# Optimization experiments

Measured on AMD Instinct MI355X. Metric: run time of the kernel, lower is better.

Reference implementation:

```python
import jax, jax.numpy as jnp
import numpy as np

T, H, I, E, TOP_K = 4096, 2048, 1024, 16, 2
I_SHARED = 1024  # moe_intermediate_size * n_shared_experts


def _silu_and_mul(gu):
    g, u = jnp.split(gu, 2, axis=-1)
    return jax.nn.silu(g) * u


def setup_inputs() -> dict:
    key = jax.random.key(0)
    ks = jax.random.split(key, 8)
    s = 0.02
    return {
        "hidden_states": jax.random.normal(ks[0], (T, H), jnp.float32),
        "gate_w": jax.random.normal(ks[1], (E, H), jnp.float32) * s,          # router
        "w1": jax.random.normal(ks[2], (E, 2 * I, H), jnp.float32) * s,       # expert gate_up
        "b1": jax.random.normal(ks[3], (E, 2 * I), jnp.float32) * s,
        "w2": jax.random.normal(ks[4], (E, H, I), jnp.float32) * s,           # expert down
        "sg_w": jax.random.normal(ks[5], (2 * I_SHARED, H), jnp.float32) * s, # shared gate_up
        "sg_b": jax.random.normal(ks[6], (2 * I_SHARED,), jnp.float32) * s,
        "sd_w": jax.random.normal(ks[7], (H, I_SHARED), jnp.float32) * s,     # shared down
    }


def reference(hidden_states, gate_w, w1, b1, w2, sg_w, sg_b, sd_w):
    x = hidden_states  # [T, H]

    # shared expert MLP (gate_up has bias, down does not)
    shared = _silu_and_mul(x @ sg_w.T + sg_b) @ sd_w.T  # [T, H]

    # router: softmax -> top-k -> renormalize (norm_topk_prob=True)
    probs = jax.nn.softmax(x @ gate_w.T, axis=-1)       # [T, E]
    wts, idx = jax.lax.top_k(probs, TOP_K)              # [T, k]
    wts = wts / jnp.sum(wts, axis=-1, keepdims=True)

    # per-expert combine coefficient: coef[e, t] = sum_k wts[t,k] * (idx[t,k]==e)
    coef = jnp.sum(jax.nn.one_hot(idx, E, dtype=x.dtype) * wts[..., None], axis=1).T  # [E, T]

    def body(acc, params):
        w1e, b1e, w2e, ce = params
        a = _silu_and_mul(x @ w1e.T + b1e)   # [T, I]
        return acc + ce[:, None] * (a @ w2e.T), None

    out, _ = jax.lax.scan(body, jnp.zeros_like(x), (w1, b1, w2, coef))
    return out + shared
```

## Files before the change

### kernel.cpp

```cpp
#include <hip/hip_runtime.h>
#include <hip/hip_bf16.h>
#include <stdint.h>

#define T_TOK 4096
#define H_DIM 2048
#define I_DIM 1024
#define NEXP  16
#define NROWS 16384

typedef short bf16x8 __attribute__((ext_vector_type(8)));
typedef float f32x4  __attribute__((ext_vector_type(4)));
typedef unsigned short u16;

__device__ __forceinline__ u16 f2b(float f) {
  union { __hip_bfloat16 h; u16 u; } cv;
  cv.h = __float2bfloat16(f);
  return cv.u;
}

__device__ __forceinline__ void gload16(const void* g, void* l) {
  __builtin_amdgcn_global_load_lds((const __attribute__((address_space(1))) void*)g,
                                   (__attribute__((address_space(3))) void*)l, 16, 0, 0);
}

__device__ __forceinline__ bf16x8 cvt_frag2(const float* pLo, const float* pHi) {
  f32x4 v0 = *(const f32x4*)pLo;
  f32x4 v1 = *(const f32x4*)pHi;
  bf16x8 o;
  o[0] = (short)f2b(v0[0]); o[1] = (short)f2b(v0[1]);
  o[2] = (short)f2b(v0[2]); o[3] = (short)f2b(v0[3]);
  o[4] = (short)f2b(v1[0]); o[5] = (short)f2b(v1[1]);
  o[6] = (short)f2b(v1[2]); o[7] = (short)f2b(v1[3]);
  return o;
}

__global__ __launch_bounds__(256) void router_kernel(const float* __restrict__ x,
                                                     const float* __restrict__ gw,
                                                     int* __restrict__ sel,
                                                     float* __restrict__ selw,
                                                     int* __restrict__ counts,
                                                     u16* __restrict__ x_bf) {
  int t = blockIdx.x;
  int tid = threadIdx.x;
  const float* xr = x + (size_t)t * H_DIM;
  double p[NEXP];
#pragma unroll
  for (int e = 0; e < NEXP; ++e) p[e] = 0.0;
  bf16x8 xs;
#pragma unroll
  for (int j = 0; j < 8; ++j) {
    int h = tid * 8 + j;
    float xf = xr[h];
    xs[j] = (short)f2b(xf);
    double xv = (double)xf;
#pragma unroll
    for (int e = 0; e < NEXP; ++e) p[e] += xv * (double)gw[e * H_DIM + h];
  }
  *(bf16x8*)(x_bf + (size_t)t * H_DIM + tid * 8) = xs;
#pragma unroll
  for (int e = 0; e < NEXP; ++e) {
#pragma unroll
    for (int off = 32; off > 0; off >>= 1) p[e] += __shfl_down(p[e], off);
  }
  __shared__ double sm[4][NEXP];
  int w = tid >> 6;
  if ((tid & 63) == 0) {
#pragma unroll
    for (int e = 0; e < NEXP; ++e) sm[w][e] = p[e];
  }
  __syncthreads();
  if (tid == 0) {
    double l0 = -1e300, l1 = -1e300;
    int e0 = 0, e1 = 0;
    for (int e = 0; e < NEXP; ++e) {
      double v = sm[0][e] + sm[1][e] + sm[2][e] + sm[3][e];
      if (v > l0) { l1 = l0; e1 = e0; l0 = v; e0 = e; }
      else if (v > l1) { l1 = v; e1 = e; }
    }
    double w0 = 1.0 / (1.0 + exp(l1 - l0));
    sel[t * 2 + 0] = e0;
    sel[t * 2 + 1] = e1;
    selw[t * 2 + 0] = (float)w0;
    selw[t * 2 + 1] = (float)(1.0 - w0);
    atomicAdd(&counts[e0], 1);
    atomicAdd(&counts[e1], 1);
  }
}

__global__ void prefix_kernel(const int* __restrict__ counts, int* __restrict__ rowbase) {
  if (threadIdx.x == 0 && blockIdx.x == 0) {
    int acc = 0;
    for (int e = 0; e < NEXP; ++e) {
      rowbase[e] = acc;
      acc += (counts[e] + 127) & ~127;
    }
    rowbase[NEXP] = acc;
  }
}

__global__ __launch_bounds__(256) void scatter_kernel(const int* __restrict__ sel,
                                                      const float* __restrict__ selw,
                                                      const int* __restrict__ rowbase,
                                                      int* __restrict__ cursor,
                                                      int* __restrict__ tok_of_row,
                                                      float* __restrict__ coef_of_row) {
  int idx = blockIdx.x * 256 + threadIdx.x;
  if (idx < T_TOK * 2) {
    int t = idx >> 1;
    int e = sel[idx];
    int slot = atomicAdd(&cursor[e], 1);
    int row = rowbase[e] + slot;
    tok_of_row[row] = t;
    coef_of_row[row] = selw[idx];
  } else if (idx < T_TOK * 3) {
    int t = idx - T_TOK * 2;
    int sb = rowbase[NEXP];
    tok_of_row[sb + t] = t;
    coef_of_row[sb + t] = 1.0f;
  }
}


__global__ __launch_bounds__(256, 3) void gemm1_kernel(
    const u16* __restrict__ x_bf, const float* __restrict__ w1,
    const float* __restrict__ sg_w,
    const float* __restrict__ b1, const float* __restrict__ sg_b,
    const int* __restrict__ tok_of_row, const int* __restrict__ counts,
    const int* __restrict__ rowbase, u16* __restrict__ abuf) {
  int nt = blockIdx.x, rt = blockIdx.y, e = blockIdx.z;
  int n_e = (e < NEXP) ? counts[e] : T_TOK;
  if (rt * 128 >= n_e) return;
  int rbase = rowbase[e];
  int n_valid = n_e - rt * 128;
  if (n_valid > 128) n_valid = 128;

  __shared__ short As[128 * 64];
  __shared__ float Bsf[128 * 64];
  __shared__ int Ts[128];

  int tid = threadIdx.x;
  if (tid < 128)
    Ts[tid] = (rt * 128 + tid < n_e) ? tok_of_row[rbase + rt * 128 + tid] : 0;
  __syncthreads();

  int wavebase = tid & 0xC0;
  const u16* srcA[4];
  short* dstA[4];
#pragma unroll
  for (int p = 0; p < 4; ++p) {
    int c = p * 256 + tid;
    int r = c >> 3;
    int koff = ((c & 7) * 8) ^ ((r & 7) << 3);
    int tok = Ts[r];
    srcA[p] = x_bf + (size_t)tok * H_DIM + koff;
    dstA[p] = &As[(p * 256 + wavebase) * 8];
  }
  const float* Wexp = (e < NEXP) ? (w1 + (size_t)e * (2 * I_DIM) * H_DIM) : sg_w;
  const float* srcB[8];
  float* dstB[8];
#pragma unroll
  for (int p = 0; p < 8; ++p) {
    int c = p * 256 + tid;
    int r = c >> 4;
    int eoff = ((c & 15) ^ (r & 15)) * 4;
    int gr = (r < 64) ? (nt * 64 + r) : (I_DIM + nt * 64 + (r - 64));
    srcB[p] = Wexp + (size_t)gr * H_DIM + eoff;
    dstB[p] = &Bsf[(p * 256 + wavebase) * 4];
  }

  f32x4 acc[4][4];
#pragma unroll
  for (int m = 0; m < 4; ++m)
#pragma unroll
    for (int n = 0; n < 4; ++n) acc[m][n] = (f32x4){0.f, 0.f, 0.f, 0.f};

  int lane = tid & 63, w = tid >> 6, wr = w >> 1, wc = w & 1;
  int laneq = lane & 15, hi = lane >> 4;

  for (int kt = 0; kt < H_DIM / 64; ++kt) {
    if (kt) __syncthreads();
#pragma unroll
    for (int p = 0; p < 4; ++p) gload16(srcA[p] + kt * 64, dstA[p]);
#pragma unroll
    for (int p = 0; p < 8; ++p) gload16(srcB[p] + kt * 64, dstB[p]);
    __syncthreads();
#pragma unroll
    for (int ks = 0; ks < 2; ++ks) {
      bf16x8 a[4], b[4];
#pragma unroll
      for (int f = 0; f < 4; ++f) {
        int rowA = wr * 64 + f * 16 + laneq;
        a[f] = *(const bf16x8*)(As + rowA * 64 + ((ks * 32 + hi * 8) ^ ((rowA & 7) << 3)));
        int rowB = ((f < 2) ? (wc * 32 + f * 16) : (64 + wc * 32 + (f - 2) * 16)) + laneq;
        int s0 = (ks * 8 + hi * 2) ^ (rowB & 15);
        const float* pB = Bsf + rowB * 64;
        b[f] = cvt_frag2(pB + s0 * 4, pB + (s0 ^ 1) * 4);
      }
#pragma unroll
      for (int f = 0; f < 4; ++f)
#pragma unroll
        for (int fn = 0; fn < 4; ++fn)
          acc[f][fn] = __builtin_amdgcn_mfma_f32_16x16x32_bf16(a[f], b[fn], acc[f][fn], 0, 0, 0);
    }
  }

  const float* bias = (e < NEXP) ? (b1 + (size_t)e * (2 * I_DIM)) : sg_b;
#pragma unroll
  for (int nf = 0; nf < 2; ++nf) {
    int j = nt * 64 + wc * 32 + nf * 16 + laneq;
    float bg = bias[j];
    float bu = bias[I_DIM + j];
#pragma unroll
    for (int mf = 0; mf < 4; ++mf) {
#pragma unroll
      for (int reg = 0; reg < 4; ++reg) {
        int r = wr * 64 + mf * 16 + hi * 4 + reg;
        if (r < n_valid) {
          float g = acc[mf][nf][reg] + bg;
          float u = acc[mf][nf + 2][reg] + bu;
          float s = g / (1.0f + __expf(-g));
          abuf[(size_t)(rbase + rt * 128 + r) * I_DIM + j] = f2b(s * u);
        }
      }
    }
  }
}

__global__ __launch_bounds__(256, 3) void gemm2_kernel(
    const u16* __restrict__ abuf, const float* __restrict__ w2,
    const float* __restrict__ sd_w,
    const int* __restrict__ tok_of_row, const float* __restrict__ coef_of_row,
    const int* __restrict__ counts, const int* __restrict__ rowbase,
    float* __restrict__ out) {
  int nt = blockIdx.x, rt = blockIdx.y, e = blockIdx.z;
  int n_e = (e < NEXP) ? counts[e] : T_TOK;
  if (rt * 128 >= n_e) return;
  int rbase = rowbase[e];
  int n_valid = n_e - rt * 128;
  if (n_valid > 128) n_valid = 128;

  __shared__ short As[128 * 64];
  __shared__ float Bsf[128 * 64];
  __shared__ int Ts[128];
  __shared__ float Cs[128];

  int tid = threadIdx.x;
  if (tid < 128) {
    bool valid = rt * 128 + tid < n_e;
    int row = rbase + rt * 128 + tid;
    Ts[tid] = valid ? tok_of_row[row] : 0;
    Cs[tid] = valid ? coef_of_row[row] : 0.0f;
  }
  __syncthreads();

  int wavebase = tid & 0xC0;
  const u16* srcA[4];
  short* dstA[4];
#pragma unroll
  for (int p = 0; p < 4; ++p) {
    int c = p * 256 + tid;
    int r = c >> 3;
    int koff = ((c & 7) * 8) ^ ((r & 7) << 3);
    srcA[p] = abuf + (size_t)(rbase + rt * 128 + r) * I_DIM + koff;
    dstA[p] = &As[(p * 256 + wavebase) * 8];
  }
  const float* Wexp = (e < NEXP) ? (w2 + (size_t)e * H_DIM * I_DIM) : sd_w;
  const float* srcB[8];
  float* dstB[8];
#pragma unroll
  for (int p = 0; p < 8; ++p) {
    int c = p * 256 + tid;
    int r = c >> 4;
    int eoff = ((c & 15) ^ (r & 15)) * 4;
    srcB[p] = Wexp + (size_t)(nt * 128 + r) * I_DIM + eoff;
    dstB[p] = &Bsf[(p * 256 + wavebase) * 4];
  }

  f32x4 acc[4][4];
#pragma unroll
  for (int m = 0; m < 4; ++m)
#pragma unroll
    for (int n = 0; n < 4; ++n) acc[m][n] = (f32x4){0.f, 0.f, 0.f, 0.f};

  int lane = tid & 63, w = tid >> 6, wr = w >> 1, wc = w & 1;
  int laneq = lane & 15, hi = lane >> 4;

  for (int kt = 0; kt < I_DIM / 64; ++kt) {
    if (kt) __syncthreads();
#pragma unroll
    for (int p = 0; p < 4; ++p) gload16(srcA[p] + kt * 64, dstA[p]);
#pragma unroll
    for (int p = 0; p < 8; ++p) gload16(srcB[p] + kt * 64, dstB[p]);
    __syncthreads();
#pragma unroll
    for (int ks = 0; ks < 2; ++ks) {
      bf16x8 a[4], b[4];
#pragma unroll
      for (int f = 0; f < 4; ++f) {
        int rowA = wr * 64 + f * 16 + laneq;
        int rowB = wc * 64 + f * 16 + laneq;
        a[f] = *(const bf16x8*)(As + rowA * 64 + ((ks * 32 + hi * 8) ^ ((rowA & 7) << 3)));
        int s0 = (ks * 8 + hi * 2) ^ (rowB & 15);
        const float* pB = Bsf + rowB * 64;
        b[f] = cvt_frag2(pB + s0 * 4, pB + (s0 ^ 1) * 4);
      }
#pragma unroll
      for (int f = 0; f < 4; ++f)
#pragma unroll
        for (int fn = 0; fn < 4; ++fn)
          acc[f][fn] = __builtin_amdgcn_mfma_f32_16x16x32_bf16(a[f], b[fn], acc[f][fn], 0, 0, 0);
    }
  }

#pragma unroll
  for (int mf = 0; mf < 4; ++mf) {
#pragma unroll
    for (int nf = 0; nf < 4; ++nf) {
      int col = nt * 128 + wc * 64 + nf * 16 + laneq;
#pragma unroll
      for (int reg = 0; reg < 4; ++reg) {
        int r = wr * 64 + mf * 16 + hi * 4 + reg;
        if (r < n_valid) {
          int tok = Ts[r];
          atomicAdd(out + (size_t)tok * H_DIM + col, acc[mf][nf][reg] * Cs[r]);
        }
      }
    }
  }
}

extern "C" void kernel_launch(void* const* d_in, const int* in_sizes, int n_in,
                              void* d_out, int out_size, void* d_ws, size_t ws_size,
                              hipStream_t stream) {
  const float* x    = (const float*)d_in[0];
  const float* gate_w = (const float*)d_in[1];
  const float* w1   = (const float*)d_in[2];
  const float* b1   = (const float*)d_in[3];
  const float* w2   = (const float*)d_in[4];
  const float* sg_w = (const float*)d_in[5];
  const float* sg_b = (const float*)d_in[6];
  const float* sd_w = (const float*)d_in[7];
  float* out = (float*)d_out;

  uint8_t* ws = (uint8_t*)d_ws;
  size_t off = 0;
  auto alloc = [&](size_t bytes) -> void* {
    void* p = ws + off;
    off += (bytes + 255) & ~(size_t)255;
    return p;
  };
  u16*  x_bf  = (u16*)alloc((size_t)T_TOK * H_DIM * 2);
  u16*  abuf  = (u16*)alloc((size_t)NROWS * I_DIM * 2);
  int*  tok_of_row  = (int*)alloc((size_t)NROWS * 4);
  float* coef_of_row = (float*)alloc((size_t)NROWS * 4);
  int*  sel   = (int*)alloc((size_t)T_TOK * 2 * 4);
  float* selw = (float*)alloc((size_t)T_TOK * 2 * 4);
  int*  counts  = (int*)alloc(256);
  int*  cursor  = (int*)alloc(256);
  int*  rowbase = (int*)alloc(256);
  (void)ws_size; (void)in_sizes; (void)n_in; (void)out_size;

  hipMemsetAsync(counts, 0, 512, stream);
  hipMemsetAsync(out, 0, (size_t)T_TOK * H_DIM * 4, stream);

  router_kernel<<<dim3(T_TOK), dim3(256), 0, stream>>>(x, gate_w, sel, selw, counts, x_bf);
  prefix_kernel<<<dim3(1), dim3(64), 0, stream>>>(counts, rowbase);
  scatter_kernel<<<dim3(48), dim3(256), 0, stream>>>(sel, selw, rowbase, cursor, tok_of_row, coef_of_row);

  gemm1_kernel<<<dim3(16, 32, 17), dim3(256), 0, stream>>>(
      x_bf, w1, sg_w, b1, sg_b, tok_of_row, counts, rowbase, abuf);

  gemm2_kernel<<<dim3(16, 32, 17), dim3(256), 0, stream>>>(
      abuf, w2, sd_w, tok_of_row, coef_of_row, counts, rowbase, out);
}
```

Before: 469.4 us.

## Load A fragments directly from global into registers, dropping A LDS staging

Both grouped GEMM kernels stop staging the activation tile in shared memory. Each lane now reads its MFMA A fragments straight from global memory into registers, and only the fp32 weight tile still goes through LDS. Freeing the A shared buffer lets the launch-bound occupancy hint rise from 3 to 4 blocks per CU. The cost is that A rows are read redundantly by the two column waves, with uncoalesced 16-byte per-lane loads from gathered token rows, and these loads are exposed to latency before the barrier. Register pressure also rises.

```diff
diff --git a/kernel.cpp b/kernel.cpp
--- a/kernel.cpp
+++ b/kernel.cpp
@@ -121,7 +121,7 @@
 }
 
 
-__global__ __launch_bounds__(256, 3) void gemm1_kernel(
+__global__ __launch_bounds__(256, 4) void gemm1_kernel(
     const u16* __restrict__ x_bf, const float* __restrict__ w1,
     const float* __restrict__ sg_w,
     const float* __restrict__ b1, const float* __restrict__ sg_b,
@@ -134,7 +134,6 @@
   int n_valid = n_e - rt * 128;
   if (n_valid > 128) n_valid = 128;
 
-  __shared__ short As[128 * 64];
   __shared__ float Bsf[128 * 64];
   __shared__ int Ts[128];
 
@@ -143,18 +142,17 @@
     Ts[tid] = (rt * 128 + tid < n_e) ? tok_of_row[rbase + rt * 128 + tid] : 0;
   __syncthreads();
 
+  int lane = tid & 63, w = tid >> 6, wr = w >> 1, wc = w & 1;
+  int laneq = lane & 15, hi = lane >> 4;
   int wavebase = tid & 0xC0;
-  const u16* srcA[4];
-  short* dstA[4];
-#pragma unroll
-  for (int p = 0; p < 4; ++p) {
-    int c = p * 256 + tid;
-    int r = c >> 3;
-    int koff = ((c & 7) * 8) ^ ((r & 7) << 3);
-    int tok = Ts[r];
-    srcA[p] = x_bf + (size_t)tok * H_DIM + koff;
-    dstA[p] = &As[(p * 256 + wavebase) * 8];
-  }
+
+  const u16* aptr[4];
+#pragma unroll
+  for (int f = 0; f < 4; ++f) {
+    int rowA = wr * 64 + f * 16 + laneq;
+    aptr[f] = x_bf + (size_t)Ts[rowA] * H_DIM + hi * 8;
+  }
+
   const float* Wexp = (e < NEXP) ? (w1 + (size_t)e * (2 * I_DIM) * H_DIM) : sg_w;
   const float* srcB[8];
   float* dstB[8];
@@ -174,23 +172,22 @@
 #pragma unroll
     for (int n = 0; n < 4; ++n) acc[m][n] = (f32x4){0.f, 0.f, 0.f, 0.f};
 
-  int lane = tid & 63, w = tid >> 6, wr = w >> 1, wc = w & 1;
-  int laneq = lane & 15, hi = lane >> 4;
-
   for (int kt = 0; kt < H_DIM / 64; ++kt) {
     if (kt) __syncthreads();
 #pragma unroll
-    for (int p = 0; p < 4; ++p) gload16(srcA[p] + kt * 64, dstA[p]);
-#pragma unroll
     for (int p = 0; p < 8; ++p) gload16(srcB[p] + kt * 64, dstB[p]);
+    bf16x8 a[4][2];
+#pragma unroll
+    for (int f = 0; f < 4; ++f)
+#pragma unroll
+      for (int ks = 0; ks < 2; ++ks)
+        a[f][ks] = *(const bf16x8*)(aptr[f] + kt * 64 + ks * 32);
     __syncthreads();
 #pragma unroll
     for (int ks = 0; ks < 2; ++ks) {
-      bf16x8 a[4], b[4];
+      bf16x8 b[4];
 #pragma unroll
       for (int f = 0; f < 4; ++f) {
-        int rowA = wr * 64 + f * 16 + laneq;
-        a[f] = *(const bf16x8*)(As + rowA * 64 + ((ks * 32 + hi * 8) ^ ((rowA & 7) << 3)));
         int rowB = ((f < 2) ? (wc * 32 + f * 16) : (64 + wc * 32 + (f - 2) * 16)) + laneq;
         int s0 = (ks * 8 + hi * 2) ^ (rowB & 15);
         const float* pB = Bsf + rowB * 64;
@@ -200,7 +197,7 @@
       for (int f = 0; f < 4; ++f)
 #pragma unroll
         for (int fn = 0; fn < 4; ++fn)
-          acc[f][fn] = __builtin_amdgcn_mfma_f32_16x16x32_bf16(a[f], b[fn], acc[f][fn], 0, 0, 0);
+          acc[f][fn] = __builtin_amdgcn_mfma_f32_16x16x32_bf16(a[f][ks], b[fn], acc[f][fn], 0, 0, 0);
     }
   }
 
@@ -226,7 +223,7 @@
   }
 }
 
-__global__ __launch_bounds__(256, 3) void gemm2_kernel(
+__global__ __launch_bounds__(256, 4) void gemm2_kernel(
     const u16* __restrict__ abuf, const float* __restrict__ w2,
     const float* __restrict__ sd_w,
     const int* __restrict__ tok_of_row, const float* __restrict__ coef_of_row,
@@ -239,7 +236,6 @@
   int n_valid = n_e - rt * 128;
   if (n_valid > 128) n_valid = 128;
 
-  __shared__ short As[128 * 64];
   __shared__ float Bsf[128 * 64];
   __shared__ int Ts[128];
   __shared__ float Cs[128];
@@ -253,17 +249,17 @@
   }
   __syncthreads();
 
+  int lane = tid & 63, w = tid >> 6, wr = w >> 1, wc = w & 1;
+  int laneq = lane & 15, hi = lane >> 4;
   int wavebase = tid & 0xC0;
-  const u16* srcA[4];
-  short* dstA[4];
-#pragma unroll
-  for (int p = 0; p < 4; ++p) {
-    int c = p * 256 + tid;
-    int r = c >> 3;
-    int koff = ((c & 7) * 8) ^ ((r & 7) << 3);
-    srcA[p] = abuf + (size_t)(rbase + rt * 128 + r) * I_DIM + koff;
-    dstA[p] = &As[(p * 256 + wavebase) * 8];
-  }
+
+  const u16* aptr[4];
+#pragma unroll
+  for (int f = 0; f < 4; ++f) {
+    int rowA = wr * 64 + f * 16 + laneq;
+    aptr[f] = abuf + (size_t)(rbase + rt * 128 + rowA) * I_DIM + hi * 8;
+  }
+
   const float* Wexp = (e < NEXP) ? (w2 + (size_t)e * H_DIM * I_DIM) : sd_w;
   const float* srcB[8];
   float* dstB[8];
@@ -282,24 +278,23 @@
 #pragma unroll
     for (int n = 0; n < 4; ++n) acc[m][n] = (f32x4){0.f, 0.f, 0.f, 0.f};
 
-  int lane = tid & 63, w = tid >> 6, wr = w >> 1, wc = w & 1;
-  int laneq = lane & 15, hi = lane >> 4;
-
   for (int kt = 0; kt < I_DIM / 64; ++kt) {
     if (kt) __syncthreads();
 #pragma unroll
-    for (int p = 0; p < 4; ++p) gload16(srcA[p] + kt * 64, dstA[p]);
-#pragma unroll
     for (int p = 0; p < 8; ++p) gload16(srcB[p] + kt * 64, dstB[p]);
+    bf16x8 a[4][2];
+#pragma unroll
+    for (int f = 0; f < 4; ++f)
+#pragma unroll
+      for (int ks = 0; ks < 2; ++ks)
+        a[f][ks] = *(const bf16x8*)(aptr[f] + kt * 64 + ks * 32);
     __syncthreads();
 #pragma unroll
     for (int ks = 0; ks < 2; ++ks) {
-      bf16x8 a[4], b[4];
+      bf16x8 b[4];
 #pragma unroll
       for (int f = 0; f < 4; ++f) {
-        int rowA = wr * 64 + f * 16 + laneq;
         int rowB = wc * 64 + f * 16 + laneq;
-        a[f] = *(const bf16x8*)(As + rowA * 64 + ((ks * 32 + hi * 8) ^ ((rowA & 7) << 3)));
         int s0 = (ks * 8 + hi * 2) ^ (rowB & 15);
         const float* pB = Bsf + rowB * 64;
         b[f] = cvt_frag2(pB + s0 * 4, pB + (s0 ^ 1) * 4);
@@ -308,7 +303,7 @@
       for (int f = 0; f < 4; ++f)
 #pragma unroll
         for (int fn = 0; fn < 4; ++fn)
-          acc[f][fn] = __builtin_amdgcn_mfma_f32_16x16x32_bf16(a[f], b[fn], acc[f][fn], 0, 0, 0);
+          acc[f][fn] = __builtin_amdgcn_mfma_f32_16x16x32_bf16(a[f][ks], b[fn], acc[f][fn], 0, 0, 0);
     }
   }
 
```

Measured after the change: 989.2 us. 2.11x slower.

## Replace atomic scatter-add in down GEMM with per-row buffer and combine kernel

Applied to the files above, without the earlier changes.

The down-projection GEMM now writes each routed row's weighted result to a dense per-row fp32 buffer, and the shared-expert rows write directly into the output. A new combine kernel gathers each token's two expert rows and adds them into the output. This removes the fp32 global atomics and the output memset. In exchange it adds a 128 MB intermediate buffer write and read and one extra kernel launch. Correctness depends on the shared-expert tiles having fully written the output before the combine kernel runs.

```diff
diff --git a/kernel.cpp b/kernel.cpp
--- a/kernel.cpp
+++ b/kernel.cpp
@@ -103,7 +103,8 @@
                                                       const int* __restrict__ rowbase,
                                                       int* __restrict__ cursor,
                                                       int* __restrict__ tok_of_row,
-                                                      float* __restrict__ coef_of_row) {
+                                                      float* __restrict__ coef_of_row,
+                                                      int* __restrict__ row_of_tok) {
   int idx = blockIdx.x * 256 + threadIdx.x;
   if (idx < T_TOK * 2) {
     int t = idx >> 1;
@@ -112,6 +113,7 @@
     int row = rowbase[e] + slot;
     tok_of_row[row] = t;
     coef_of_row[row] = selw[idx];
+    row_of_tok[idx] = row;
   } else if (idx < T_TOK * 3) {
     int t = idx - T_TOK * 2;
     int sb = rowbase[NEXP];
@@ -231,7 +233,7 @@
     const float* __restrict__ sd_w,
     const int* __restrict__ tok_of_row, const float* __restrict__ coef_of_row,
     const int* __restrict__ counts, const int* __restrict__ rowbase,
-    float* __restrict__ out) {
+    float* __restrict__ y, float* __restrict__ out) {
   int nt = blockIdx.x, rt = blockIdx.y, e = blockIdx.z;
   int n_e = (e < NEXP) ? counts[e] : T_TOK;
   if (rt * 128 >= n_e) return;
@@ -321,11 +323,34 @@
       for (int reg = 0; reg < 4; ++reg) {
         int r = wr * 64 + mf * 16 + hi * 4 + reg;
         if (r < n_valid) {
-          int tok = Ts[r];
-          atomicAdd(out + (size_t)tok * H_DIM + col, acc[mf][nf][reg] * Cs[r]);
+          float val = acc[mf][nf][reg] * Cs[r];
+          if (e < NEXP)
+            y[(size_t)(rbase + rt * 128 + r) * H_DIM + col] = val;
+          else
+            out[(size_t)Ts[r] * H_DIM + col] = val;
         }
       }
     }
+  }
+}
+
+__global__ __launch_bounds__(256) void combine_kernel(float* __restrict__ out,
+                                                      const float* __restrict__ y,
+                                                      const int* __restrict__ row_of_tok) {
+  int t = blockIdx.x;
+  int r0 = row_of_tok[t * 2];
+  int r1 = row_of_tok[t * 2 + 1];
+  const float* y0 = y + (size_t)r0 * H_DIM;
+  const float* y1 = y + (size_t)r1 * H_DIM;
+  float* o = out + (size_t)t * H_DIM;
+  int c = threadIdx.x * 8;
+#pragma unroll
+  for (int h = 0; h < 2; ++h) {
+    float4 ov = *(float4*)(o + c + h * 4);
+    float4 a = *(const float4*)(y0 + c + h * 4);
+    float4 b = *(const float4*)(y1 + c + h * 4);
+    ov.x += a.x + b.x; ov.y += a.y + b.y; ov.z += a.z + b.z; ov.w += a.w + b.w;
+    *(float4*)(o + c + h * 4) = ov;
   }
 }
 
@@ -351,8 +376,10 @@
   };
   u16*  x_bf  = (u16*)alloc((size_t)T_TOK * H_DIM * 2);
   u16*  abuf  = (u16*)alloc((size_t)NROWS * I_DIM * 2);
+  float* y    = (float*)alloc((size_t)NROWS * H_DIM * 4);
   int*  tok_of_row  = (int*)alloc((size_t)NROWS * 4);
   float* coef_of_row = (float*)alloc((size_t)NROWS * 4);
+  int*  row_of_tok  = (int*)alloc((size_t)T_TOK * 2 * 4);
   int*  sel   = (int*)alloc((size_t)T_TOK * 2 * 4);
   float* selw = (float*)alloc((size_t)T_TOK * 2 * 4);
   int*  counts  = (int*)alloc(256);
@@ -361,15 +388,17 @@
   (void)ws_size; (void)in_sizes; (void)n_in; (void)out_size;
 
   hipMemsetAsync(counts, 0, 512, stream);
-  hipMemsetAsync(out, 0, (size_t)T_TOK * H_DIM * 4, stream);
 
   router_kernel<<<dim3(T_TOK), dim3(256), 0, stream>>>(x, gate_w, sel, selw, counts, x_bf);
   prefix_kernel<<<dim3(1), dim3(64), 0, stream>>>(counts, rowbase);
-  scatter_kernel<<<dim3(48), dim3(256), 0, stream>>>(sel, selw, rowbase, cursor, tok_of_row, coef_of_row);
+  scatter_kernel<<<dim3(48), dim3(256), 0, stream>>>(sel, selw, rowbase, cursor,
+                                                     tok_of_row, coef_of_row, row_of_tok);
 
   gemm1_kernel<<<dim3(16, 32, 17), dim3(256), 0, stream>>>(
       x_bf, w1, sg_w, b1, sg_b, tok_of_row, counts, rowbase, abuf);
 
   gemm2_kernel<<<dim3(16, 32, 17), dim3(256), 0, stream>>>(
-      abuf, w2, sd_w, tok_of_row, coef_of_row, counts, rowbase, out);
-}
+      abuf, w2, sd_w, tok_of_row, coef_of_row, counts, rowbase, y, out);
+
+  combine_kernel<<<dim3(T_TOK), dim3(256), 0, stream>>>(out, y, row_of_tok);
+}
```

New measurement: 458.2 us. 1.02x faster.
